# Kernel optimization log

Hardware: AMD Instinct MI355X
Metric: run time of the kernel (lower is better)

## Reference

```python
import jax, jax.numpy as jnp
import numpy as np

B, N, NFEAT, NHID, NOUT, H = 16, 1024, 128, 256, 256, 4
DH = NOUT // H  # 64 per head
EPS = 1e-5
ALPHA = 0.2  # LeakyReLU negative slope


def setup_inputs() -> dict:
    key = jax.random.key(0)
    ks = jax.random.split(key, 8)
    stdv = 1.0 / np.sqrt(NHID)
    return {
        "x": jax.random.normal(ks[0], (B, N, NFEAT), dtype=jnp.float32),
        "adj": jax.random.uniform(ks[1], (N, N), dtype=jnp.float32) / N,
        "gc_w": jax.random.uniform(ks[2], (NFEAT, NHID), minval=-stdv, maxval=stdv, dtype=jnp.float32),
        "gc_b": jax.random.uniform(ks[3], (NHID,), minval=-stdv, maxval=stdv, dtype=jnp.float32),
        "bn1_gamma": jnp.ones((NHID,), jnp.float32),
        "bn1_beta": jnp.zeros((NHID,), jnp.float32),
        "gat_w": jax.random.normal(ks[4], (H, NHID, DH), dtype=jnp.float32) * (1.0 / np.sqrt(NHID)),
        "conv_w": jax.random.normal(ks[5], (NOUT, NOUT, 3), dtype=jnp.float32) * (1.0 / np.sqrt(NOUT * 3)),
        "conv_b": jnp.zeros((NOUT,), jnp.float32),
        "bn2_gamma": jnp.ones((NOUT,), jnp.float32),
        "bn2_beta": jnp.zeros((NOUT,), jnp.float32),
    }


def reference(x, adj, gc_w, gc_b, bn1_gamma, bn1_beta, gat_w, conv_w, conv_b, bn2_gamma, bn2_beta):
    # --- GraphConvolution: adj @ (x @ W) + b, relu ---
    h = jnp.einsum("bnf,fo->bno", x, gc_w)
    h = jnp.einsum("nm,bmo->bno", adj, h) + gc_b
    h = jax.nn.relu(h)
    # --- BatchNorm1d over channel dim (training-mode batch stats), relu ---
    mu = h.mean((0, 1))
    var = h.var((0, 1))
    h = (h - mu) * jax.lax.rsqrt(var + EPS) * bn1_gamma + bn1_beta
    h = jax.nn.relu(h)
    # --- Multi-head GAT: per head hp, e = hp hp^T, leakyrelu, softmax, attn @ hp ---
    hp = jnp.einsum("bnf,hfd->bhnd", h, gat_w)          # (B,H,N,DH)
    e = jnp.einsum("bhnd,bhmd->bhnm", hp, hp)            # (B,H,N,N)
    e = jnp.where(e > 0, e, ALPHA * e)
    attn = jax.nn.softmax(e, axis=-1)
    out = jnp.einsum("bhnm,bhmd->bhnd", attn, hp)        # = sum_m attn * hp (the B,N,N,d repeat in torch)
    out = out.transpose(0, 2, 1, 3).reshape(B, N, H * DH)  # concat heads -> (B,N,NOUT)
    # --- TCN block: conv1d (k=3, pad 1) over node axis, batchnorm, relu (dropout=eval) ---
    xc = out.transpose(0, 2, 1)                          # (B,C,N)
    y = jax.lax.conv_general_dilated(xc, conv_w, (1,), [(1, 1)],
                                     dimension_numbers=("NCH", "OIH", "NCH"))
    y = y + conv_b[None, :, None]
    mu2 = y.mean((0, 2), keepdims=True)
    var2 = y.var((0, 2), keepdims=True)
    y = (y - mu2) * jax.lax.rsqrt(var2 + EPS) * bn2_gamma[None, :, None] + bn2_beta[None, :, None]
    y = jax.nn.relu(y)
    return y.transpose(0, 2, 1)                          # (B,N,NOUT)
```

## Files before the change

kernel.cpp:

```cpp
#include <hip/hip_runtime.h>
#include <hip/hip_bf16.h>


typedef unsigned short u16;
typedef __attribute__((ext_vector_type(8))) short short8;
typedef __attribute__((ext_vector_type(4))) float f32x4;

static __device__ __forceinline__ float4 ld4(const float* p){ return *(const float4*)p; }
static __device__ __forceinline__ void st4(float* p, float4 v){ *(float4*)p = v; }

static __device__ __forceinline__ u16 f2bf(float f){
  unsigned u = __builtin_bit_cast(unsigned, f);
  unsigned r = u + 0x7FFFu + ((u >> 16) & 1u);
  return (u16)(r >> 16);
}
static __device__ __forceinline__ float bf2f(u16 h){
  unsigned u = ((unsigned)h) << 16; return __builtin_bit_cast(float, u);
}
static __device__ __forceinline__ void st4bf(u16* p, u16 a, u16 b, u16 c, u16 d){
  uint2 v; v.x = (unsigned)a | ((unsigned)b << 16); v.y = (unsigned)c | ((unsigned)d << 16);
  *(uint2*)p = v;
}
static __device__ __forceinline__ f32x4 mfma16(short8 a, short8 b, f32x4 c){
  return __builtin_amdgcn_mfma_f32_16x16x32_bf16(a, b, c, 0, 0, 0);
}

template<int SPLIT, int K, int NN, int MODE>
static __device__ __forceinline__ void mgemm_body(
    const u16* __restrict__ Ah_, const u16* __restrict__ Al_,
    const u16* __restrict__ Bh_, const u16* __restrict__ Bl_,
    const u16* __restrict__ zbuf,
    void* __restrict__ C0v, void* __restrict__ C1v, void* __restrict__ C2v,
    const float* __restrict__ bias)
{
  constexpr int KT = K / 32;
  __shared__ u16 Ah[4096], Bh[4096];
  __shared__ u16 Al[SPLIT == 3 ? 4096 : 8], Bl[SPLIT == 3 ? 4096 : 8];
  const int tid = threadIdx.x;
  const int n0 = blockIdx.x * 128, m0 = blockIdx.y * 128;
  const int lane = tid & 63, l15 = lane & 15, lq = lane >> 4;
  const int w = tid >> 6, wr = w >> 1, wc = w & 1;

  f32x4 acc[4][4] = {};

  for (int kt = 0; kt < KT; ++kt){
    const int k0 = kt * 32;
#pragma unroll
    for (int r = 0; r < 2; ++r){
      const int slot = r * 256 + tid;
      const int row = slot & 127, kh = slot >> 7;
      const int ldsoff = (r * 256 + (tid & 192)) * 8;
      const u16* asrc;
      if constexpr (MODE == 3){
        const int kz = k0 >> 8;
        const int ci0 = (k0 & 255) + kh * 8;
        const int R = m0 + row;
        const int nn = (R & 1023) + kz - 1;
        asrc = ((unsigned)nn < 1024u) ? (Ah_ + (size_t)(R + kz - 1) * 256 + ci0) : zbuf;
      } else {
        asrc = Ah_ + (size_t)(m0 + row) * K + k0 + kh * 8;
      }
      __builtin_amdgcn_global_load_lds(asrc, &Ah[ldsoff], 16, 0, 0);
      const u16* bsrc = Bh_ + (size_t)(n0 + row) * K + k0 + kh * 8;
      __builtin_amdgcn_global_load_lds(bsrc, &Bh[ldsoff], 16, 0, 0);
      if constexpr (SPLIT == 3){
        const u16* asrc2 = Al_ + (size_t)(m0 + row) * K + k0 + kh * 8;
        __builtin_amdgcn_global_load_lds(asrc2, &Al[ldsoff], 16, 0, 0);
        const u16* bsrc2 = Bl_ + (size_t)(n0 + row) * K + k0 + kh * 8;
        __builtin_amdgcn_global_load_lds(bsrc2, &Bl[ldsoff], 16, 0, 0);
      }
    }
    __syncthreads();
    short8 afh[4], bfh[4], afl[4], bfl[4];
#pragma unroll
    for (int f = 0; f < 4; ++f){
      afh[f] = *(const short8*)&Ah[(lq * 128 + wr * 64 + f * 16 + l15) * 8];
      bfh[f] = *(const short8*)&Bh[(lq * 128 + wc * 64 + f * 16 + l15) * 8];
      if constexpr (SPLIT == 3){
        afl[f] = *(const short8*)&Al[(lq * 128 + wr * 64 + f * 16 + l15) * 8];
        bfl[f] = *(const short8*)&Bl[(lq * 128 + wc * 64 + f * 16 + l15) * 8];
      }
    }
#pragma unroll
    for (int fi = 0; fi < 4; ++fi)
#pragma unroll
      for (int fj = 0; fj < 4; ++fj){
        acc[fi][fj] = mfma16(afh[fi], bfh[fj], acc[fi][fj]);
        if constexpr (SPLIT == 3){
          acc[fi][fj] = mfma16(afl[fi], bfh[fj], acc[fi][fj]);
          acc[fi][fj] = mfma16(afh[fi], bfl[fj], acc[fi][fj]);
        }
      }
    __syncthreads();
  }

  const int rb = m0 + wr * 64;
  const int cb = n0 + wc * 64;
  if constexpr (MODE == 0){
    u16* H = (u16*)C0v; u16* L = (u16*)C1v;
#pragma unroll
    for (int fi = 0; fi < 4; ++fi){
      const int R = rb + fi * 16 + lq * 4;
      const int nn = R & 1023, bq = R >> 10;
#pragma unroll
      for (int fj = 0; fj < 4; ++fj){
        const int c = cb + fj * 16 + l15;
        const size_t off = (size_t)(bq * 256 + c) * 1024 + nn;
        u16 h_[4], l_[4];
#pragma unroll
        for (int r = 0; r < 4; ++r){
          float v = acc[fi][fj][r];
          u16 hi = f2bf(v); h_[r] = hi; l_[r] = f2bf(v - bf2f(hi));
        }
        st4bf(H + off, h_[0], h_[1], h_[2], h_[3]);
        st4bf(L + off, l_[0], l_[1], l_[2], l_[3]);
      }
    }
  } else if constexpr (MODE == 1){
    float* G = (float*)C0v;
#pragma unroll
    for (int fj = 0; fj < 4; ++fj){
      const int c = cb + fj * 16 + l15;
      const int o = c & 255, bq = c >> 8;
      const float bs = bias[o];
#pragma unroll
      for (int fi = 0; fi < 4; ++fi){
        const int R = rb + fi * 16 + lq * 4;
#pragma unroll
        for (int r = 0; r < 4; ++r)
          G[((size_t)bq * 1024 + R + r) * 256 + o] = fmaxf(acc[fi][fj][r] + bs, 0.f);
      }
    }
  } else if constexpr (MODE == 2){
    u16* H = (u16*)C0v; u16* L = (u16*)C1v; u16* T = (u16*)C2v;
#pragma unroll
    for (int fi = 0; fi < 4; ++fi){
      const int R = rb + fi * 16 + lq * 4;
#pragma unroll
      for (int fj = 0; fj < 4; ++fj){
        const int c = cb + fj * 16 + l15;
        u16 h_[4];
#pragma unroll
        for (int r = 0; r < 4; ++r){
          float v = acc[fi][fj][r];
          u16 hi = f2bf(v); h_[r] = hi;
          H[(size_t)(R + r) * 256 + c] = hi;
          L[(size_t)(R + r) * 256 + c] = f2bf(v - bf2f(hi));
        }
        st4bf(T + (size_t)c * 16384 + R, h_[0], h_[1], h_[2], h_[3]);
      }
    }
  } else {
    float* Y = (float*)C0v;
#pragma unroll
    for (int fj = 0; fj < 4; ++fj){
      const int c = cb + fj * 16 + l15;
      const float bs = bias[c];
#pragma unroll
      for (int fi = 0; fi < 4; ++fi){
        const int R = rb + fi * 16 + lq * 4;
#pragma unroll
        for (int r = 0; r < 4; ++r)
          Y[(size_t)(R + r) * 256 + c] = acc[fi][fj][r] + bs;
      }
    }
  }
}

__global__ __launch_bounds__(256) void gemm0_k(
    const u16* __restrict__ Ah_, const u16* __restrict__ Bh_,
    const u16* __restrict__ zbuf, void* __restrict__ C0, void* __restrict__ C1)
{ mgemm_body<1, 128, 256, 0>(Ah_, nullptr, Bh_, nullptr, zbuf, C0, C1, nullptr, nullptr); }

__global__ __launch_bounds__(256) void gemm1_k(
    const u16* __restrict__ Ah_, const u16* __restrict__ Al_,
    const u16* __restrict__ Bh_, const u16* __restrict__ Bl_,
    const u16* __restrict__ zbuf, void* __restrict__ C0, const float* __restrict__ bias)
{ mgemm_body<3, 1024, 4096, 1>(Ah_, Al_, Bh_, Bl_, zbuf, C0, nullptr, nullptr, bias); }

__global__ __launch_bounds__(256) void gemm2_k(
    const u16* __restrict__ Ah_, const u16* __restrict__ Al_,
    const u16* __restrict__ Bh_, const u16* __restrict__ Bl_,
    const u16* __restrict__ zbuf,
    void* __restrict__ C0, void* __restrict__ C1, void* __restrict__ C2)
{ mgemm_body<3, 256, 256, 2>(Ah_, Al_, Bh_, Bl_, zbuf, C0, C1, C2, nullptr); }

__global__ __launch_bounds__(256) void gemm3_k(
    const u16* __restrict__ Ah_, const u16* __restrict__ Bh_,
    const u16* __restrict__ zbuf, void* __restrict__ C0, const float* __restrict__ bias)
{ mgemm_body<1, 768, 256, 3>(Ah_, nullptr, Bh_, nullptr, zbuf, C0, nullptr, nullptr, bias); }

__global__ __launch_bounds__(256) void flash(
    const u16* __restrict__ hp_hi, const u16* __restrict__ hp_lo,
    const u16* __restrict__ hpT, u16* __restrict__ ao)
{
  __shared__ u16 Khi[4096], Klo[4096], Vt[4096];
  __shared__ u16 Pl[4][4096];
  __shared__ float Ls[4][64];
  const int tid = threadIdx.x;
  const int lane = tid & 63, l15 = lane & 15, lq = lane >> 4, w = tid >> 6;
  const int bid = blockIdx.x;
  const int b = bid >> 4, h = (bid >> 2) & 3, qq = bid & 3;
  const size_t qrow0 = (size_t)b * 1024 + qq * 256 + w * 64;

  short8 qh[4][2], ql[4][2];
#pragma unroll
  for (int fi = 0; fi < 4; ++fi)
#pragma unroll
    for (int ks = 0; ks < 2; ++ks){
      const size_t off = (qrow0 + fi * 16 + l15) * 256 + h * 64 + ks * 32 + lq * 8;
      qh[fi][ks] = *(const short8*)(hp_hi + off);
      ql[fi][ks] = *(const short8*)(hp_lo + off);
    }

  f32x4 o_[4][4] = {};
  float ls[16] = {};

  for (int kt = 0; kt < 16; ++kt){
    const int kv0 = kt * 64;
#pragma unroll
    for (int r = 0; r < 2; ++r){
      const int slot = r * 256 + tid;
      const int g1 = slot >> 6, g2 = slot & 63;
      const int ldsoff = (r * 256 + (tid & 192)) * 8;
      const u16* ksrc = hp_hi + ((size_t)b * 1024 + kv0 + g2) * 256 + h * 64 + g1 * 8;
      __builtin_amdgcn_global_load_lds(ksrc, &Khi[ldsoff], 16, 0, 0);
      const u16* ksrc2 = hp_lo + ((size_t)b * 1024 + kv0 + g2) * 256 + h * 64 + g1 * 8;
      __builtin_amdgcn_global_load_lds(ksrc2, &Klo[ldsoff], 16, 0, 0);
      const u16* vsrc = hpT + (size_t)(h * 64 + g2) * 16384 + b * 1024 + kv0 + g1 * 8;
      __builtin_amdgcn_global_load_lds(vsrc, &Vt[ldsoff], 16, 0, 0);
    }
    __syncthreads();

#pragma unroll
    for (int nf = 0; nf < 4; ++nf){
      short8 kf[2], kg[2];
#pragma unroll
      for (int ks = 0; ks < 2; ++ks){
        kf[ks] = *(const short8*)&Khi[((ks * 4 + lq) * 64 + nf * 16 + l15) * 8];
        kg[ks] = *(const short8*)&Klo[((ks * 4 + lq) * 64 + nf * 16 + l15) * 8];
      }
      const int kv = nf * 16 + l15;
#pragma unroll
      for (int mf = 0; mf < 4; ++mf){
        f32x4 s = {};
#pragma unroll
        for (int ks = 0; ks < 2; ++ks){
          s = mfma16(qh[mf][ks], kf[ks], s);
          s = mfma16(ql[mf][ks], kf[ks], s);
          s = mfma16(qh[mf][ks], kg[ks], s);
        }
        const int qb = mf * 16 + lq * 4;
        const int base = ((kv >> 3) * 64 + qb) * 8 + (kv & 7);
#pragma unroll
        for (int r = 0; r < 4; ++r){
          float v = s[r];
          v = v > 0.f ? v : 0.2f * v;
          const float p = __expf(v - 40.f);
          ls[mf * 4 + r] += p;
          Pl[w][base + r * 8] = f2bf(p);
        }
      }
    }

#pragma unroll
    for (int ks = 0; ks < 2; ++ks){
      short8 va[4], pf[4];
#pragma unroll
      for (int f = 0; f < 4; ++f){
        va[f] = *(const short8*)&Vt[((ks * 4 + lq) * 64 + f * 16 + l15) * 8];
        pf[f] = *(const short8*)&Pl[w][((ks * 4 + lq) * 64 + f * 16 + l15) * 8];
      }
#pragma unroll
      for (int df = 0; df < 4; ++df)
#pragma unroll
        for (int qf = 0; qf < 4; ++qf)
          o_[df][qf] = mfma16(va[df], pf[qf], o_[df][qf]);
    }
    __syncthreads();
  }

#pragma unroll
  for (int mask = 1; mask < 16; mask <<= 1)
#pragma unroll
    for (int i = 0; i < 16; ++i)
      ls[i] += __shfl_xor(ls[i], mask, 64);
  if (l15 == 0){
#pragma unroll
    for (int mf = 0; mf < 4; ++mf)
#pragma unroll
      for (int r = 0; r < 4; ++r)
        Ls[w][mf * 16 + lq * 4 + r] = ls[mf * 4 + r];
  }
  __syncthreads();
  float inv[4];
#pragma unroll
  for (int qf = 0; qf < 4; ++qf) inv[qf] = 1.0f / Ls[w][qf * 16 + l15];

#pragma unroll
  for (int qf = 0; qf < 4; ++qf)
#pragma unroll
    for (int df = 0; df < 4; ++df){
      const size_t addr = (qrow0 + qf * 16 + l15) * 256 + h * 64 + df * 16 + lq * 4;
      st4bf(ao + addr,
            f2bf(o_[df][qf][0] * inv[qf]), f2bf(o_[df][qf][1] * inv[qf]),
            f2bf(o_[df][qf][2] * inv[qf]), f2bf(o_[df][qf][3] * inv[qf]));
    }
}

__global__ __launch_bounds__(256) void bn_partial(const float* __restrict__ buf,
                                                  float* __restrict__ part)
{
  const int bi = blockIdx.x, t = threadIdx.x;
  const float* p = buf + (size_t)bi * 64 * 256 + t;
  float s = 0.f, q = 0.f;
#pragma unroll 4
  for (int r = 0; r < 64; ++r){ const float v = p[(size_t)r * 256]; s += v; q = fmaf(v, v, q); }
  part[bi * 512 + t] = s;
  part[bi * 512 + 256 + t] = q;
}

__global__ __launch_bounds__(256) void bn_final(const float* __restrict__ part,
                                                const float* __restrict__ gamma,
                                                const float* __restrict__ beta,
                                                float* __restrict__ prm)
{
  const int t = threadIdx.x;
  float s = 0.f, q = 0.f;
#pragma unroll 8
  for (int i = 0; i < 256; ++i){ s += part[i * 512 + t]; q += part[i * 512 + 256 + t]; }
  const float mu = s * (1.f / 16384.f);
  const float var = q * (1.f / 16384.f) - mu * mu;
  prm[t] = mu;
  prm[256 + t] = rsqrtf(var + 1e-5f) * gamma[t];
  prm[512 + t] = beta[t];
}

__global__ __launch_bounds__(256) void bn_apply_split(const float* __restrict__ in,
    u16* __restrict__ H, u16* __restrict__ L, const float* __restrict__ prm)
{
  const int idx = blockIdx.x * 256 + threadIdx.x;
  const size_t off = (size_t)idx * 4;
  const int o = (int)(off & 255);
  const float4 x = ld4(in + off);
  const float4 m = ld4(prm + o), rs = ld4(prm + 256 + o), bt = ld4(prm + 512 + o);
  u16 h_[4], l_[4];
  float v;
  v = fmaxf(fmaf(x.x - m.x, rs.x, bt.x), 0.f); h_[0] = f2bf(v); l_[0] = f2bf(v - bf2f(h_[0]));
  v = fmaxf(fmaf(x.y - m.y, rs.y, bt.y), 0.f); h_[1] = f2bf(v); l_[1] = f2bf(v - bf2f(h_[1]));
  v = fmaxf(fmaf(x.z - m.z, rs.z, bt.z), 0.f); h_[2] = f2bf(v); l_[2] = f2bf(v - bf2f(h_[2]));
  v = fmaxf(fmaf(x.w - m.w, rs.w, bt.w), 0.f); h_[3] = f2bf(v); l_[3] = f2bf(v - bf2f(h_[3]));
  st4bf(H + off, h_[0], h_[1], h_[2], h_[3]);
  st4bf(L + off, l_[0], l_[1], l_[2], l_[3]);
}

__global__ __launch_bounds__(256) void bn_apply(const float* __restrict__ in,
                                                float* __restrict__ outp,
                                                const float* __restrict__ prm)
{
  const int idx = blockIdx.x * 256 + threadIdx.x;
  const size_t off = (size_t)idx * 8;
  const int o = (int)(off & 255);
  const float4 x0 = ld4(in + off),      x1 = ld4(in + off + 4);
  const float4 m0 = ld4(prm + o),       m1 = ld4(prm + o + 4);
  const float4 r0 = ld4(prm + 256 + o), r1 = ld4(prm + 256 + o + 4);
  const float4 b0 = ld4(prm + 512 + o), b1 = ld4(prm + 512 + o + 4);
  float4 y0, y1;
  y0.x = fmaxf(fmaf(x0.x - m0.x, r0.x, b0.x), 0.f);
  y0.y = fmaxf(fmaf(x0.y - m0.y, r0.y, b0.y), 0.f);
  y0.z = fmaxf(fmaf(x0.z - m0.z, r0.z, b0.z), 0.f);
  y0.w = fmaxf(fmaf(x0.w - m0.w, r0.w, b0.w), 0.f);
  y1.x = fmaxf(fmaf(x1.x - m1.x, r1.x, b1.x), 0.f);
  y1.y = fmaxf(fmaf(x1.y - m1.y, r1.y, b1.y), 0.f);
  y1.z = fmaxf(fmaf(x1.z - m1.z, r1.z, b1.z), 0.f);
  y1.w = fmaxf(fmaf(x1.w - m1.w, r1.w, b1.w), 0.f);
  st4(outp + off, y0);
  st4(outp + off + 4, y1);
}

__global__ __launch_bounds__(256) void pack_w(
    const float* __restrict__ x, const float* __restrict__ adj,
    const float* __restrict__ gcw, const float* __restrict__ gatw,
    const float* __restrict__ convw,
    u16* __restrict__ xbf, u16* __restrict__ adjh, u16* __restrict__ adjl,
    u16* __restrict__ w0t, u16* __restrict__ w2th, u16* __restrict__ w2tl,
    u16* __restrict__ cwt, u16* __restrict__ zb)
{
  const int idx = blockIdx.x * 256 + threadIdx.x;
  if (idx < 2097152) xbf[idx] = f2bf(x[idx]);
  if (idx < 1048576){
    const float v = adj[idx];
    const u16 hi = f2bf(v);
    adjh[idx] = hi; adjl[idx] = f2bf(v - bf2f(hi));
  }
  if (idx < 32768){
    const int o = idx >> 7, f = idx & 127;
    w0t[idx] = f2bf(gcw[f * 256 + o]);
  }
  if (idx < 65536){
    const int c = idx >> 8, f = idx & 255;
    const float v = gatw[(c >> 6) * 16384 + f * 64 + (c & 63)];
    const u16 hi = f2bf(v);
    w2th[idx] = hi; w2tl[idx] = f2bf(v - bf2f(hi));
  }
  if (idx < 196608){
    const int co = idx / 768, k = idx - co * 768;
    const int kz = k >> 8, ci = k & 255;
    cwt[idx] = f2bf(convw[co * 768 + ci * 3 + kz]);
  }
  if (idx < 2048) zb[idx] = 0;
}

extern "C" void kernel_launch(void* const* d_in, const int* in_sizes, int n_in,
                              void* d_out, int out_size, void* d_ws, size_t ws_size,
                              hipStream_t stream)
{
  const float* x     = (const float*)d_in[0];
  const float* adj   = (const float*)d_in[1];
  const float* gc_w  = (const float*)d_in[2];
  const float* gc_b  = (const float*)d_in[3];
  const float* bn1g  = (const float*)d_in[4];
  const float* bn1b  = (const float*)d_in[5];
  const float* gatw  = (const float*)d_in[6];
  const float* convw = (const float*)d_in[7];
  const float* convb = (const float*)d_in[8];
  const float* bn2g  = (const float*)d_in[9];
  const float* bn2b  = (const float*)d_in[10];
  char* ws  = (char*)d_ws;
  char* out = (char*)d_out;

  u16* h1t_hi = (u16*)(ws + 0);
  u16* h1t_lo = (u16*)(ws + 8388608);
  u16* x_bf   = (u16*)(ws + 16777216);
  u16* adj_hi = (u16*)(ws + 20971520);
  u16* adj_lo = (u16*)(ws + 23068672);
  u16* hpT    = (u16*)(ws + 16777216);
  u16* w0t    = (u16*)(ws + 25165824);
  u16* w2th   = (u16*)(ws + 25231360);
  u16* w2tl   = (u16*)(ws + 25362432);
  u16* cwt    = (u16*)(ws + 25493504);
  u16* zbuf   = (u16*)(ws + 25886720);
  float* P1   = (float*)(ws + 25890816);
  float* PR1  = (float*)(ws + 26415104);
  float* PR2  = (float*)(ws + 26419200);
  u16* h_hi  = (u16*)(ws + 0);
  u16* h_lo  = (u16*)(ws + 8388608);
  u16* ao    = (u16*)(ws + 0);
  float* g   = (float*)out;
  u16* hp_hi = (u16*)out;
  u16* hp_lo = (u16*)(out + 8388608);
  float* y   = (float*)out;

  pack_w<<<8192, 256, 0, stream>>>(x, adj, gc_w, gatw, convw,
                                   x_bf, adj_hi, adj_lo, w0t, w2th, w2tl, cwt, zbuf);
  gemm0_k<<<dim3(2, 128), 256, 0, stream>>>(x_bf, w0t, zbuf, h1t_hi, h1t_lo);
  gemm1_k<<<dim3(32, 8), 256, 0, stream>>>(adj_hi, adj_lo, h1t_hi, h1t_lo, zbuf, g, gc_b);
  bn_partial<<<256, 256, 0, stream>>>(g, P1);
  bn_final<<<1, 256, 0, stream>>>(P1, bn1g, bn1b, PR1);
  bn_apply_split<<<4096, 256, 0, stream>>>(g, h_hi, h_lo, PR1);
  gemm2_k<<<dim3(2, 128), 256, 0, stream>>>(h_hi, h_lo, w2th, w2tl, zbuf, hp_hi, hp_lo, hpT);
  flash<<<256, 256, 0, stream>>>(hp_hi, hp_lo, hpT, ao);
  gemm3_k<<<dim3(2, 128), 256, 0, stream>>>(ao, cwt, zbuf, y, convb);
  bn_partial<<<256, 256, 0, stream>>>(y, P1);
  bn_final<<<1, 256, 0, stream>>>(P1, bn2g, bn2b, PR2);
  bn_apply<<<2048, 256, 0, stream>>>(y, y, PR2);
}
```

Before: 338.8 us.

## Halve flash query tile to double grid and swap gemm1 block order

The attention kernel now gives each wave 32 query rows instead of 64 and launches 512 blocks instead of 256. Consecutive blocks now walk over batches rather than heads and query chunks. This is meant to fill all compute units on the MI355X and raise occupancy by using fewer registers and less LDS per block. The cost is that K/V tiles are reloaded twice as often across blocks. Separately, gemm1 swaps its grid axes so that consecutive blocks share the same A row-block, which should improve L2 reuse of the adjacency matrix.

```diff
diff --git a/kernel.cpp b/kernel.cpp
--- a/kernel.cpp
+++ b/kernel.cpp
@@ -25,7 +25,7 @@
   return __builtin_amdgcn_mfma_f32_16x16x32_bf16(a, b, c, 0, 0, 0);
 }
 
-template<int SPLIT, int K, int NN, int MODE>
+template<int SPLIT, int K, int NN, int MODE, int AXSWAP>
 static __device__ __forceinline__ void mgemm_body(
     const u16* __restrict__ Ah_, const u16* __restrict__ Al_,
     const u16* __restrict__ Bh_, const u16* __restrict__ Bl_,
@@ -37,7 +37,8 @@
   __shared__ u16 Ah[4096], Bh[4096];
   __shared__ u16 Al[SPLIT == 3 ? 4096 : 8], Bl[SPLIT == 3 ? 4096 : 8];
   const int tid = threadIdx.x;
-  const int n0 = blockIdx.x * 128, m0 = blockIdx.y * 128;
+  const int n0 = (AXSWAP ? blockIdx.y : blockIdx.x) * 128;
+  const int m0 = (AXSWAP ? blockIdx.x : blockIdx.y) * 128;
   const int lane = tid & 63, l15 = lane & 15, lq = lane >> 4;
   const int w = tid >> 6, wr = w >> 1, wc = w & 1;
 
@@ -170,51 +171,51 @@
 __global__ __launch_bounds__(256) void gemm0_k(
     const u16* __restrict__ Ah_, const u16* __restrict__ Bh_,
     const u16* __restrict__ zbuf, void* __restrict__ C0, void* __restrict__ C1)
-{ mgemm_body<1, 128, 256, 0>(Ah_, nullptr, Bh_, nullptr, zbuf, C0, C1, nullptr, nullptr); }
+{ mgemm_body<1, 128, 256, 0, 0>(Ah_, nullptr, Bh_, nullptr, zbuf, C0, C1, nullptr, nullptr); }
 
 __global__ __launch_bounds__(256) void gemm1_k(
     const u16* __restrict__ Ah_, const u16* __restrict__ Al_,
     const u16* __restrict__ Bh_, const u16* __restrict__ Bl_,
     const u16* __restrict__ zbuf, void* __restrict__ C0, const float* __restrict__ bias)
-{ mgemm_body<3, 1024, 4096, 1>(Ah_, Al_, Bh_, Bl_, zbuf, C0, nullptr, nullptr, bias); }
+{ mgemm_body<3, 1024, 4096, 1, 1>(Ah_, Al_, Bh_, Bl_, zbuf, C0, nullptr, nullptr, bias); }
 
 __global__ __launch_bounds__(256) void gemm2_k(
     const u16* __restrict__ Ah_, const u16* __restrict__ Al_,
     const u16* __restrict__ Bh_, const u16* __restrict__ Bl_,
     const u16* __restrict__ zbuf,
     void* __restrict__ C0, void* __restrict__ C1, void* __restrict__ C2)
-{ mgemm_body<3, 256, 256, 2>(Ah_, Al_, Bh_, Bl_, zbuf, C0, C1, C2, nullptr); }
+{ mgemm_body<3, 256, 256, 2, 0>(Ah_, Al_, Bh_, Bl_, zbuf, C0, C1, C2, nullptr); }
 
 __global__ __launch_bounds__(256) void gemm3_k(
     const u16* __restrict__ Ah_, const u16* __restrict__ Bh_,
     const u16* __restrict__ zbuf, void* __restrict__ C0, const float* __restrict__ bias)
-{ mgemm_body<1, 768, 256, 3>(Ah_, nullptr, Bh_, nullptr, zbuf, C0, nullptr, nullptr, bias); }
+{ mgemm_body<1, 768, 256, 3, 0>(Ah_, nullptr, Bh_, nullptr, zbuf, C0, nullptr, nullptr, bias); }
 
 __global__ __launch_bounds__(256) void flash(
     const u16* __restrict__ hp_hi, const u16* __restrict__ hp_lo,
     const u16* __restrict__ hpT, u16* __restrict__ ao)
 {
   __shared__ u16 Khi[4096], Klo[4096], Vt[4096];
-  __shared__ u16 Pl[4][4096];
-  __shared__ float Ls[4][64];
+  __shared__ u16 Pl[4][2048];
+  __shared__ float Ls[4][32];
   const int tid = threadIdx.x;
   const int lane = tid & 63, l15 = lane & 15, lq = lane >> 4, w = tid >> 6;
   const int bid = blockIdx.x;
-  const int b = bid >> 4, h = (bid >> 2) & 3, qq = bid & 3;
-  const size_t qrow0 = (size_t)b * 1024 + qq * 256 + w * 64;
-
-  short8 qh[4][2], ql[4][2];
-#pragma unroll
-  for (int fi = 0; fi < 4; ++fi)
+  const int b = bid & 15, k_ = bid >> 4, h = k_ >> 3, qo = k_ & 7;
+  const size_t qrow0 = (size_t)b * 1024 + qo * 128 + w * 32;
+
+  short8 qh[2][2], ql[2][2];
+#pragma unroll
+  for (int mf = 0; mf < 2; ++mf)
 #pragma unroll
     for (int ks = 0; ks < 2; ++ks){
-      const size_t off = (qrow0 + fi * 16 + l15) * 256 + h * 64 + ks * 32 + lq * 8;
-      qh[fi][ks] = *(const short8*)(hp_hi + off);
-      ql[fi][ks] = *(const short8*)(hp_lo + off);
-    }
-
-  f32x4 o_[4][4] = {};
-  float ls[16] = {};
+      const size_t off = (qrow0 + mf * 16 + l15) * 256 + h * 64 + ks * 32 + lq * 8;
+      qh[mf][ks] = *(const short8*)(hp_hi + off);
+      ql[mf][ks] = *(const short8*)(hp_lo + off);
+    }
+
+  f32x4 o_[4][2] = {};
+  float ls[8] = {};
 
   for (int kt = 0; kt < 16; ++kt){
     const int kv0 = kt * 64;
@@ -242,7 +243,7 @@
       }
       const int kv = nf * 16 + l15;
 #pragma unroll
-      for (int mf = 0; mf < 4; ++mf){
+      for (int mf = 0; mf < 2; ++mf){
         f32x4 s = {};
 #pragma unroll
         for (int ks = 0; ks < 2; ++ks){
@@ -251,7 +252,7 @@
           s = mfma16(qh[mf][ks], kg[ks], s);
         }
         const int qb = mf * 16 + lq * 4;
-        const int base = ((kv >> 3) * 64 + qb) * 8 + (kv & 7);
+        const int base = ((kv >> 3) * 32 + qb) * 8 + (kv & 7);
 #pragma unroll
         for (int r = 0; r < 4; ++r){
           float v = s[r];
@@ -265,16 +266,17 @@
 
 #pragma unroll
     for (int ks = 0; ks < 2; ++ks){
-      short8 va[4], pf[4];
-#pragma unroll
-      for (int f = 0; f < 4; ++f){
+      short8 va[4], pf[2];
+#pragma unroll
+      for (int f = 0; f < 4; ++f)
         va[f] = *(const short8*)&Vt[((ks * 4 + lq) * 64 + f * 16 + l15) * 8];
-        pf[f] = *(const short8*)&Pl[w][((ks * 4 + lq) * 64 + f * 16 + l15) * 8];
-      }
+#pragma unroll
+      for (int f = 0; f < 2; ++f)
+        pf[f] = *(const short8*)&Pl[w][((ks * 4 + lq) * 32 + f * 16 + l15) * 8];
 #pragma unroll
       for (int df = 0; df < 4; ++df)
 #pragma unroll
-        for (int qf = 0; qf < 4; ++qf)
+        for (int qf = 0; qf < 2; ++qf)
           o_[df][qf] = mfma16(va[df], pf[qf], o_[df][qf]);
     }
     __syncthreads();
@@ -283,22 +285,22 @@
 #pragma unroll
   for (int mask = 1; mask < 16; mask <<= 1)
 #pragma unroll
-    for (int i = 0; i < 16; ++i)
+    for (int i = 0; i < 8; ++i)
       ls[i] += __shfl_xor(ls[i], mask, 64);
   if (l15 == 0){
 #pragma unroll
-    for (int mf = 0; mf < 4; ++mf)
+    for (int mf = 0; mf < 2; ++mf)
 #pragma unroll
       for (int r = 0; r < 4; ++r)
         Ls[w][mf * 16 + lq * 4 + r] = ls[mf * 4 + r];
   }
   __syncthreads();
-  float inv[4];
-#pragma unroll
-  for (int qf = 0; qf < 4; ++qf) inv[qf] = 1.0f / Ls[w][qf * 16 + l15];
-
-#pragma unroll
-  for (int qf = 0; qf < 4; ++qf)
+  float inv[2];
+#pragma unroll
+  for (int qf = 0; qf < 2; ++qf) inv[qf] = 1.0f / Ls[w][qf * 16 + l15];
+
+#pragma unroll
+  for (int qf = 0; qf < 2; ++qf)
 #pragma unroll
     for (int df = 0; df < 4; ++df){
       const size_t addr = (qrow0 + qf * 16 + l15) * 256 + h * 64 + df * 16 + lq * 4;
@@ -454,12 +456,12 @@
   pack_w<<<8192, 256, 0, stream>>>(x, adj, gc_w, gatw, convw,
                                    x_bf, adj_hi, adj_lo, w0t, w2th, w2tl, cwt, zbuf);
   gemm0_k<<<dim3(2, 128), 256, 0, stream>>>(x_bf, w0t, zbuf, h1t_hi, h1t_lo);
-  gemm1_k<<<dim3(32, 8), 256, 0, stream>>>(adj_hi, adj_lo, h1t_hi, h1t_lo, zbuf, g, gc_b);
+  gemm1_k<<<dim3(8, 32), 256, 0, stream>>>(adj_hi, adj_lo, h1t_hi, h1t_lo, zbuf, g, gc_b);
   bn_partial<<<256, 256, 0, stream>>>(g, P1);
   bn_final<<<1, 256, 0, stream>>>(P1, bn1g, bn1b, PR1);
   bn_apply_split<<<4096, 256, 0, stream>>>(g, h_hi, h_lo, PR1);
   gemm2_k<<<dim3(2, 128), 256, 0, stream>>>(h_hi, h_lo, w2th, w2tl, zbuf, hp_hi, hp_lo, hpT);
-  flash<<<256, 256, 0, stream>>>(hp_hi, hp_lo, hpT, ao);
+  flash<<<512, 256, 0, stream>>>(hp_hi, hp_lo, hpT, ao);
   gemm3_k<<<dim3(2, 128), 256, 0, stream>>>(ao, cwt, zbuf, y, convb);
   bn_partial<<<256, 256, 0, stream>>>(y, P1);
   bn_final<<<1, 256, 0, stream>>>(P1, bn2g, bn2b, PR2);
```

Result: faster. 321.6 us (-5.1%).

## Shrink GEMM and flash-attention tiles to launch more blocks across CUs

Applied to the files above, without the earlier changes.

The shared GEMM template now takes its block-tile and warp-grid shape as parameters. Three GEMMs move to 128x64 tiles and the adj GEMM to 64x128 tiles with swapped grid axes, so grids grow from 256 to 512 blocks. The flash-attention kernel drops from 64 to 16 query rows per warp, growing its grid from 256 to 1024 blocks and cutting per-wave registers and LDS. The aim is better occupancy and CU fill on a 256-CU part. In exchange, K/V tiles are reloaded by more blocks and each block does less MFMA work per LDS load.

```diff
diff --git a/kernel.cpp b/kernel.cpp
--- a/kernel.cpp
+++ b/kernel.cpp
@@ -25,7 +25,7 @@
   return __builtin_amdgcn_mfma_f32_16x16x32_bf16(a, b, c, 0, 0, 0);
 }
 
-template<int SPLIT, int K, int NN, int MODE>
+template<int SPLIT, int K, int NN, int MODE, int AXSWAP, int BM, int BN, int WR, int WC>
 static __device__ __forceinline__ void mgemm_body(
     const u16* __restrict__ Ah_, const u16* __restrict__ Al_,
     const u16* __restrict__ Bh_, const u16* __restrict__ Bl_,
@@ -34,21 +34,24 @@
     const float* __restrict__ bias)
 {
   constexpr int KT = K / 32;
-  __shared__ u16 Ah[4096], Bh[4096];
-  __shared__ u16 Al[SPLIT == 3 ? 4096 : 8], Bl[SPLIT == 3 ? 4096 : 8];
+  constexpr int WM = BM / WR, WN = BN / WC;
+  constexpr int MI = WM / 16, NJ = WN / 16;
+  __shared__ u16 Ah[BM * 32], Bh[BN * 32];
+  __shared__ u16 Al[SPLIT == 3 ? BM * 32 : 8], Bl[SPLIT == 3 ? BN * 32 : 8];
   const int tid = threadIdx.x;
-  const int n0 = blockIdx.x * 128, m0 = blockIdx.y * 128;
+  const int n0 = (AXSWAP ? blockIdx.y : blockIdx.x) * BN;
+  const int m0 = (AXSWAP ? blockIdx.x : blockIdx.y) * BM;
   const int lane = tid & 63, l15 = lane & 15, lq = lane >> 4;
-  const int w = tid >> 6, wr = w >> 1, wc = w & 1;
-
-  f32x4 acc[4][4] = {};
+  const int w = tid >> 6, wr = w / WC, wc = w % WC;
+
+  f32x4 acc[MI][NJ] = {};
 
   for (int kt = 0; kt < KT; ++kt){
     const int k0 = kt * 32;
 #pragma unroll
-    for (int r = 0; r < 2; ++r){
+    for (int r = 0; r < BM / 64; ++r){
       const int slot = r * 256 + tid;
-      const int row = slot & 127, kh = slot >> 7;
+      const int row = slot & (BM - 1), kh = slot / BM;
       const int ldsoff = (r * 256 + (tid & 192)) * 8;
       const u16* asrc;
       if constexpr (MODE == 3){
@@ -61,30 +64,41 @@
         asrc = Ah_ + (size_t)(m0 + row) * K + k0 + kh * 8;
       }
       __builtin_amdgcn_global_load_lds(asrc, &Ah[ldsoff], 16, 0, 0);
+      if constexpr (SPLIT == 3){
+        const u16* asrc2 = Al_ + (size_t)(m0 + row) * K + k0 + kh * 8;
+        __builtin_amdgcn_global_load_lds(asrc2, &Al[ldsoff], 16, 0, 0);
+      }
+    }
+#pragma unroll
+    for (int r = 0; r < BN / 64; ++r){
+      const int slot = r * 256 + tid;
+      const int row = slot & (BN - 1), kh = slot / BN;
+      const int ldsoff = (r * 256 + (tid & 192)) * 8;
       const u16* bsrc = Bh_ + (size_t)(n0 + row) * K + k0 + kh * 8;
       __builtin_amdgcn_global_load_lds(bsrc, &Bh[ldsoff], 16, 0, 0);
       if constexpr (SPLIT == 3){
-        const u16* asrc2 = Al_ + (size_t)(m0 + row) * K + k0 + kh * 8;
-        __builtin_amdgcn_global_load_lds(asrc2, &Al[ldsoff], 16, 0, 0);
         const u16* bsrc2 = Bl_ + (size_t)(n0 + row) * K + k0 + kh * 8;
         __builtin_amdgcn_global_load_lds(bsrc2, &Bl[ldsoff], 16, 0, 0);
       }
     }
     __syncthreads();
-    short8 afh[4], bfh[4], afl[4], bfl[4];
-#pragma unroll
-    for (int f = 0; f < 4; ++f){
-      afh[f] = *(const short8*)&Ah[(lq * 128 + wr * 64 + f * 16 + l15) * 8];
-      bfh[f] = *(const short8*)&Bh[(lq * 128 + wc * 64 + f * 16 + l15) * 8];
-      if constexpr (SPLIT == 3){
-        afl[f] = *(const short8*)&Al[(lq * 128 + wr * 64 + f * 16 + l15) * 8];
-        bfl[f] = *(const short8*)&Bl[(lq * 128 + wc * 64 + f * 16 + l15) * 8];
-      }
-    }
-#pragma unroll
-    for (int fi = 0; fi < 4; ++fi)
-#pragma unroll
-      for (int fj = 0; fj < 4; ++fj){
+    short8 afh[MI], bfh[NJ], afl[MI], bfl[NJ];
+#pragma unroll
+    for (int f = 0; f < MI; ++f){
+      afh[f] = *(const short8*)&Ah[(lq * BM + wr * WM + f * 16 + l15) * 8];
+      if constexpr (SPLIT == 3)
+        afl[f] = *(const short8*)&Al[(lq * BM + wr * WM + f * 16 + l15) * 8];
+    }
+#pragma unroll
+    for (int f = 0; f < NJ; ++f){
+      bfh[f] = *(const short8*)&Bh[(lq * BN + wc * WN + f * 16 + l15) * 8];
+      if constexpr (SPLIT == 3)
+        bfl[f] = *(const short8*)&Bl[(lq * BN + wc * WN + f * 16 + l15) * 8];
+    }
+#pragma unroll
+    for (int fi = 0; fi < MI; ++fi)
+#pragma unroll
+      for (int fj = 0; fj < NJ; ++fj){
         acc[fi][fj] = mfma16(afh[fi], bfh[fj], acc[fi][fj]);
         if constexpr (SPLIT == 3){
           acc[fi][fj] = mfma16(afl[fi], bfh[fj], acc[fi][fj]);
@@ -94,16 +108,16 @@
     __syncthreads();
   }
 
-  const int rb = m0 + wr * 64;
-  const int cb = n0 + wc * 64;
+  const int rb = m0 + wr * WM;
+  const int cb = n0 + wc * WN;
   if constexpr (MODE == 0){
     u16* H = (u16*)C0v; u16* L = (u16*)C1v;
 #pragma unroll
-    for (int fi = 0; fi < 4; ++fi){
+    for (int fi = 0; fi < MI; ++fi){
       const int R = rb + fi * 16 + lq * 4;
       const int nn = R & 1023, bq = R >> 10;
 #pragma unroll
-      for (int fj = 0; fj < 4; ++fj){
+      for (int fj = 0; fj < NJ; ++fj){
         const int c = cb + fj * 16 + l15;
         const size_t off = (size_t)(bq * 256 + c) * 1024 + nn;
         u16 h_[4], l_[4];
@@ -119,12 +133,12 @@
   } else if constexpr (MODE == 1){
     float* G = (float*)C0v;
 #pragma unroll
-    for (int fj = 0; fj < 4; ++fj){
+    for (int fj = 0; fj < NJ; ++fj){
       const int c = cb + fj * 16 + l15;
       const int o = c & 255, bq = c >> 8;
       const float bs = bias[o];
 #pragma unroll
-      for (int fi = 0; fi < 4; ++fi){
+      for (int fi = 0; fi < MI; ++fi){
         const int R = rb + fi * 16 + lq * 4;
 #pragma unroll
         for (int r = 0; r < 4; ++r)
@@ -134,10 +148,10 @@
   } else if constexpr (MODE == 2){
     u16* H = (u16*)C0v; u16* L = (u16*)C1v; u16* T = (u16*)C2v;
 #pragma unroll
-    for (int fi = 0; fi < 4; ++fi){
+    for (int fi = 0; fi < MI; ++fi){
       const int R = rb + fi * 16 + lq * 4;
 #pragma unroll
-      for (int fj = 0; fj < 4; ++fj){
+      for (int fj = 0; fj < NJ; ++fj){
         const int c = cb + fj * 16 + l15;
         u16 h_[4];
 #pragma unroll
@@ -153,11 +167,11 @@
   } else {
     float* Y = (float*)C0v;
 #pragma unroll
-    for (int fj = 0; fj < 4; ++fj){
+    for (int fj = 0; fj < NJ; ++fj){
       const int c = cb + fj * 16 + l15;
       const float bs = bias[c];
 #pragma unroll
-      for (int fi = 0; fi < 4; ++fi){
+      for (int fi = 0; fi < MI; ++fi){
         const int R = rb + fi * 16 + lq * 4;
 #pragma unroll
         for (int r = 0; r < 4; ++r)
@@ -170,51 +184,49 @@
 __global__ __launch_bounds__(256) void gemm0_k(
     const u16* __restrict__ Ah_, const u16* __restrict__ Bh_,
     const u16* __restrict__ zbuf, void* __restrict__ C0, void* __restrict__ C1)
-{ mgemm_body<1, 128, 256, 0>(Ah_, nullptr, Bh_, nullptr, zbuf, C0, C1, nullptr, nullptr); }
+{ mgemm_body<1, 128, 256, 0, 0, 128, 64, 2, 2>(Ah_, nullptr, Bh_, nullptr, zbuf, C0, C1, nullptr, nullptr); }
 
 __global__ __launch_bounds__(256) void gemm1_k(
     const u16* __restrict__ Ah_, const u16* __restrict__ Al_,
     const u16* __restrict__ Bh_, const u16* __restrict__ Bl_,
     const u16* __restrict__ zbuf, void* __restrict__ C0, const float* __restrict__ bias)
-{ mgemm_body<3, 1024, 4096, 1>(Ah_, Al_, Bh_, Bl_, zbuf, C0, nullptr, nullptr, bias); }
+{ mgemm_body<3, 1024, 4096, 1, 1, 64, 128, 1, 4>(Ah_, Al_, Bh_, Bl_, zbuf, C0, nullptr, nullptr, bias); }
 
 __global__ __launch_bounds__(256) void gemm2_k(
     const u16* __restrict__ Ah_, const u16* __restrict__ Al_,
     const u16* __restrict__ Bh_, const u16* __restrict__ Bl_,
     const u16* __restrict__ zbuf,
     void* __restrict__ C0, void* __restrict__ C1, void* __restrict__ C2)
-{ mgemm_body<3, 256, 256, 2>(Ah_, Al_, Bh_, Bl_, zbuf, C0, C1, C2, nullptr); }
+{ mgemm_body<3, 256, 256, 2, 0, 128, 64, 2, 2>(Ah_, Al_, Bh_, Bl_, zbuf, C0, C1, C2, nullptr); }
 
 __global__ __launch_bounds__(256) void gemm3_k(
     const u16* __restrict__ Ah_, const u16* __restrict__ Bh_,
     const u16* __restrict__ zbuf, void* __restrict__ C0, const float* __restrict__ bias)
-{ mgemm_body<1, 768, 256, 3>(Ah_, nullptr, Bh_, nullptr, zbuf, C0, nullptr, nullptr, bias); }
+{ mgemm_body<1, 768, 256, 3, 0, 128, 64, 2, 2>(Ah_, nullptr, Bh_, nullptr, zbuf, C0, nullptr, nullptr, bias); }
 
 __global__ __launch_bounds__(256) void flash(
     const u16* __restrict__ hp_hi, const u16* __restrict__ hp_lo,
     const u16* __restrict__ hpT, u16* __restrict__ ao)
 {
   __shared__ u16 Khi[4096], Klo[4096], Vt[4096];
-  __shared__ u16 Pl[4][4096];
-  __shared__ float Ls[4][64];
+  __shared__ u16 Pl[4][1024];
+  __shared__ float Ls[4][16];
   const int tid = threadIdx.x;
   const int lane = tid & 63, l15 = lane & 15, lq = lane >> 4, w = tid >> 6;
   const int bid = blockIdx.x;
-  const int b = bid >> 4, h = (bid >> 2) & 3, qq = bid & 3;
-  const size_t qrow0 = (size_t)b * 1024 + qq * 256 + w * 64;
-
-  short8 qh[4][2], ql[4][2];
-#pragma unroll
-  for (int fi = 0; fi < 4; ++fi)
-#pragma unroll
-    for (int ks = 0; ks < 2; ++ks){
-      const size_t off = (qrow0 + fi * 16 + l15) * 256 + h * 64 + ks * 32 + lq * 8;
-      qh[fi][ks] = *(const short8*)(hp_hi + off);
-      ql[fi][ks] = *(const short8*)(hp_lo + off);
-    }
-
-  f32x4 o_[4][4] = {};
-  float ls[16] = {};
+  const int b = bid & 15, k_ = bid >> 4, h = k_ >> 4, qo = k_ & 15;
+  const size_t qrow0 = (size_t)b * 1024 + qo * 64 + w * 16;
+
+  short8 qh[2], ql[2];
+#pragma unroll
+  for (int ks = 0; ks < 2; ++ks){
+    const size_t off = (qrow0 + l15) * 256 + h * 64 + ks * 32 + lq * 8;
+    qh[ks] = *(const short8*)(hp_hi + off);
+    ql[ks] = *(const short8*)(hp_lo + off);
+  }
+
+  f32x4 o_[4] = {};
+  float ls[4] = {};
 
   for (int kt = 0; kt < 16; ++kt){
     const int kv0 = kt * 64;
@@ -241,41 +253,34 @@
         kg[ks] = *(const short8*)&Klo[((ks * 4 + lq) * 64 + nf * 16 + l15) * 8];
       }
       const int kv = nf * 16 + l15;
-#pragma unroll
-      for (int mf = 0; mf < 4; ++mf){
-        f32x4 s = {};
-#pragma unroll
-        for (int ks = 0; ks < 2; ++ks){
-          s = mfma16(qh[mf][ks], kf[ks], s);
-          s = mfma16(ql[mf][ks], kf[ks], s);
-          s = mfma16(qh[mf][ks], kg[ks], s);
-        }
-        const int qb = mf * 16 + lq * 4;
-        const int base = ((kv >> 3) * 64 + qb) * 8 + (kv & 7);
-#pragma unroll
-        for (int r = 0; r < 4; ++r){
-          float v = s[r];
-          v = v > 0.f ? v : 0.2f * v;
-          const float p = __expf(v - 40.f);
-          ls[mf * 4 + r] += p;
-          Pl[w][base + r * 8] = f2bf(p);
-        }
+      f32x4 s = {};
+#pragma unroll
+      for (int ks = 0; ks < 2; ++ks){
+        s = mfma16(qh[ks], kf[ks], s);
+        s = mfma16(ql[ks], kf[ks], s);
+        s = mfma16(qh[ks], kg[ks], s);
+      }
+      const int base = ((kv >> 3) * 16 + lq * 4) * 8 + (kv & 7);
+#pragma unroll
+      for (int r = 0; r < 4; ++r){
+        float v = s[r];
+        v = v > 0.f ? v : 0.2f * v;
+        const float p = __expf(v - 40.f);
+        ls[r] += p;
+        Pl[w][base + r * 8] = f2bf(p);
       }
     }
 
 #pragma unroll
     for (int ks = 0; ks < 2; ++ks){
-      short8 va[4], pf[4];
-#pragma unroll
-      for (int f = 0; f < 4; ++f){
+      short8 va[4];
+#pragma unroll
+      for (int f = 0; f < 4; ++f)
         va[f] = *(const short8*)&Vt[((ks * 4 + lq) * 64 + f * 16 + l15) * 8];
-        pf[f] = *(const short8*)&Pl[w][((ks * 4 + lq) * 64 + f * 16 + l15) * 8];
-      }
+      const short8 pf = *(const short8*)&Pl[w][((ks * 4 + lq) * 16 + l15) * 8];
 #pragma unroll
       for (int df = 0; df < 4; ++df)
-#pragma unroll
-        for (int qf = 0; qf < 4; ++qf)
-          o_[df][qf] = mfma16(va[df], pf[qf], o_[df][qf]);
+        o_[df] = mfma16(va[df], pf, o_[df]);
     }
     __syncthreads();
   }
@@ -283,29 +288,22 @@
 #pragma unroll
   for (int mask = 1; mask < 16; mask <<= 1)
 #pragma unroll
-    for (int i = 0; i < 16; ++i)
+    for (int i = 0; i < 4; ++i)
       ls[i] += __shfl_xor(ls[i], mask, 64);
   if (l15 == 0){
 #pragma unroll
-    for (int mf = 0; mf < 4; ++mf)
-#pragma unroll
-      for (int r = 0; r < 4; ++r)
-        Ls[w][mf * 16 + lq * 4 + r] = ls[mf * 4 + r];
+    for (int r = 0; r < 4; ++r) Ls[w][lq * 4 + r] = ls[r];
   }
   __syncthreads();
-  float inv[4];
-#pragma unroll
-  for (int qf = 0; qf < 4; ++qf) inv[qf] = 1.0f / Ls[w][qf * 16 + l15];
-
-#pragma unroll
-  for (int qf = 0; qf < 4; ++qf)
-#pragma unroll
-    for (int df = 0; df < 4; ++df){
-      const size_t addr = (qrow0 + qf * 16 + l15) * 256 + h * 64 + df * 16 + lq * 4;
-      st4bf(ao + addr,
-            f2bf(o_[df][qf][0] * inv[qf]), f2bf(o_[df][qf][1] * inv[qf]),
-            f2bf(o_[df][qf][2] * inv[qf]), f2bf(o_[df][qf][3] * inv[qf]));
-    }
+  const float inv = 1.0f / Ls[w][l15];
+
+#pragma unroll
+  for (int df = 0; df < 4; ++df){
+    const size_t addr = (qrow0 + l15) * 256 + h * 64 + df * 16 + lq * 4;
+    st4bf(ao + addr,
+          f2bf(o_[df][0] * inv), f2bf(o_[df][1] * inv),
+          f2bf(o_[df][2] * inv), f2bf(o_[df][3] * inv));
+  }
 }
 
 __global__ __launch_bounds__(256) void bn_partial(const float* __restrict__ buf,
@@ -453,14 +451,14 @@
 
   pack_w<<<8192, 256, 0, stream>>>(x, adj, gc_w, gatw, convw,
                                    x_bf, adj_hi, adj_lo, w0t, w2th, w2tl, cwt, zbuf);
-  gemm0_k<<<dim3(2, 128), 256, 0, stream>>>(x_bf, w0t, zbuf, h1t_hi, h1t_lo);
-  gemm1_k<<<dim3(32, 8), 256, 0, stream>>>(adj_hi, adj_lo, h1t_hi, h1t_lo, zbuf, g, gc_b);
+  gemm0_k<<<dim3(4, 128), 256, 0, stream>>>(x_bf, w0t, zbuf, h1t_hi, h1t_lo);
+  gemm1_k<<<dim3(16, 32), 256, 0, stream>>>(adj_hi, adj_lo, h1t_hi, h1t_lo, zbuf, g, gc_b);
   bn_partial<<<256, 256, 0, stream>>>(g, P1);
   bn_final<<<1, 256, 0, stream>>>(P1, bn1g, bn1b, PR1);
   bn_apply_split<<<4096, 256, 0, stream>>>(g, h_hi, h_lo, PR1);
-  gemm2_k<<<dim3(2, 128), 256, 0, stream>>>(h_hi, h_lo, w2th, w2tl, zbuf, hp_hi, hp_lo, hpT);
-  flash<<<256, 256, 0, stream>>>(hp_hi, hp_lo, hpT, ao);
-  gemm3_k<<<dim3(2, 128), 256, 0, stream>>>(ao, cwt, zbuf, y, convb);
+  gemm2_k<<<dim3(4, 128), 256, 0, stream>>>(h_hi, h_lo, w2th, w2tl, zbuf, hp_hi, hp_lo, hpT);
+  flash<<<1024, 256, 0, stream>>>(hp_hi, hp_lo, hpT, ao);
+  gemm3_k<<<dim3(4, 128), 256, 0, stream>>>(ao, cwt, zbuf, y, convb);
   bn_partial<<<256, 256, 0, stream>>>(y, P1);
   bn_final<<<1, 256, 0, stream>>>(P1, bn2g, bn2b, PR2);
   bn_apply<<<2048, 256, 0, stream>>>(y, y, PR2);
```

Result: faster. 314.7 us (-7.1%).
